# Kernel tuning notes

Hardware: AMD Instinct MI355X
Metric: run time of the kernel (lower is better)

The kernel has to match this reference:

```python
import jax, jax.numpy as jnp
import numpy as np

N = 4096     # batch of positions
E = 32       # descriptor buckets (experts)
NBLK = 12    # residual blocks per head


def _ln(x, g, b, eps=1e-5):
    m = x.mean(-1, keepdims=True)
    v = ((x - m) ** 2).mean(-1, keepdims=True)
    return (x - m) / jnp.sqrt(v + eps) * g + b


def _gelu(x):
    return jax.nn.gelu(x, approximate=False)  # torch nn.GELU default = exact erf


def setup_inputs() -> dict:
    key = jax.random.key(0)
    ks = iter(jax.random.split(key, 64))

    def nrm(shape, scale=0.05):
        return jax.random.normal(next(ks), shape, jnp.float32) * scale

    return {
        "piece_idx": jax.random.randint(next(ks), (N, 64), 0, 12),
        "side_flag": jax.random.randint(next(ks), (N,), 0, 2),
        "ep_file": jax.random.randint(next(ks), (N,), 0, 8),
        "castle_ms": jax.random.uniform(next(ks), (N, 4), jnp.float32),
        "fifty_a": jax.random.uniform(next(ks), (N,), jnp.float32),
        "descriptor_index": jax.random.randint(next(ks), (N,), 0, E),
        # per-bucket embedding tables, stacked on a leading expert axis
        "Wp_w": nrm((E, 64, 12, 32)), "Wp_b": nrm((E, 64, 12, 32)),
        "Wc_w": nrm((E, 4, 32)), "Wc_b": nrm((E, 4, 32)),
        "Wep_w": nrm((E, 8, 32)), "Wep_b": nrm((E, 8, 32)),
        "Wf_w": nrm((E, 2, 32)), "Wf_b": nrm((E, 2, 32)),
        # per-bucket MLP head params (weights stored as [in,out])
        "fc1_w": nrm((E, 2240, 256)), "fc1_b": nrm((E, 256)),
        "ln1_g": jnp.ones((E, 256)), "ln1_b": jnp.zeros((E, 256)),
        "fc2_w": nrm((E, 256, 32)), "fc2_b": nrm((E, 32)),
        "ln2_g": jnp.ones((E, 32)), "ln2_b": jnp.zeros((E, 32)),
        "blkA_w": nrm((NBLK, E, 32, 32)), "blkA_b": nrm((NBLK, E, 32)),
        "blkA_g": jnp.ones((NBLK, E, 32)), "blkA_be": jnp.zeros((NBLK, E, 32)),
        "blkB_w": nrm((NBLK, E, 32, 32)), "blkB_b": nrm((NBLK, E, 32)),
        "blkB_g": jnp.ones((NBLK, E, 32)), "blkB_be": jnp.zeros((NBLK, E, 32)),
        "out_w": nrm((E, 32, 51)), "out_b": nrm((E, 51)),
        "bins": jnp.linspace(0.0, 1.0, 51),
    }


def reference(piece_idx, side_flag, ep_file, castle_ms, fifty_a, descriptor_index,
              Wp_w, Wp_b, Wc_w, Wc_b, Wep_w, Wep_b, Wf_w, Wf_b,
              fc1_w, fc1_b, ln1_g, ln1_b, fc2_w, fc2_b, ln2_g, ln2_b,
              blkA_w, blkA_b, blkA_g, blkA_be, blkB_w, blkB_b, blkB_g, blkB_be,
              out_w, out_b, bins):
    desc = descriptor_index
    side = side_flag.astype(bool)
    n = piece_idx.shape[0]

    # ---- per-bucket, side-selected embedding gathers -> x_emb [N,2240] ----
    sq = jnp.arange(64)
    pc = jnp.maximum(piece_idx, 0)                                 # clamp -1 -> 0
    w_emb = Wp_w[desc[:, None], sq[None, :], pc]                    # [N,64,32]
    b_emb = Wp_b[desc[:, None], sq[None, :], pc]
    piece_emb = jnp.where(side[:, None, None], b_emb, w_emb)
    piece_emb = piece_emb * (piece_idx >= 0)[..., None].astype(piece_emb.dtype)
    pieces_vec = piece_emb.reshape(n, 2048)

    Wc = jnp.where(side[:, None, None], Wc_b[desc], Wc_w[desc])     # [N,4,32]
    castle_vec = (castle_ms[..., None] * Wc).reshape(n, 128)

    Wep = jnp.where(side[:, None, None], Wep_b[desc], Wep_w[desc])  # [N,8,32]
    epc = jnp.maximum(ep_file, 0)
    ep_vec = jnp.take_along_axis(Wep, epc[:, None, None], axis=1)[:, 0]
    ep_vec = ep_vec * (ep_file >= 0)[:, None].astype(ep_vec.dtype)

    Wf = jnp.where(side[:, None, None], Wf_b[desc], Wf_w[desc])     # [N,2,32]
    fifty_vec = (1.0 - fifty_a)[:, None] * Wf[:, 0] + fifty_a[:, None] * Wf[:, 1]

    x = jnp.concatenate([pieces_vec, castle_vec, ep_vec, fifty_vec], axis=1)  # [N,2240]

    # ---- expert-routed dense layer: all-expert GEMM + per-token select ----
    def dense_moe(h, W, b):
        ha = jnp.einsum('nd,edh->neh', h, W)                        # [N,E,out]
        hsel = jnp.take_along_axis(ha, desc[:, None, None], axis=1)[:, 0]
        return hsel + b[desc]

    h = _ln(_gelu(dense_moe(x, fc1_w, fc1_b)), ln1_g[desc], ln1_b[desc])   # [N,256]
    h = _ln(_gelu(dense_moe(h, fc2_w, fc2_b)), ln2_g[desc], ln2_b[desc])   # [N,32]

    def blk(carry, p):
        wA, bA, gA, beA, wB, bB, gB, beB = p
        y = _ln(_gelu(dense_moe(carry, wA, bA)), gA[desc], beA[desc])
        y = _ln(_gelu(dense_moe(y, wB, bB)), gB[desc], beB[desc])
        return carry + y, None

    h, _ = jax.lax.scan(blk, h, (blkA_w, blkA_b, blkA_g, blkA_be,
                                 blkB_w, blkB_b, blkB_g, blkB_be))

    logits = dense_moe(_gelu(h), out_w, out_b)                      # [N,51]
    p_win = jnp.sum(jax.nn.softmax(logits, axis=-1) * bins, axis=-1, keepdims=True)
    return logits, p_win
```

## Files before the change

### kernel.cpp

```cpp
#include <hip/hip_runtime.h>
#include <math.h>

#define N 4096
#define E 32
#define NBLK 12
#define D_IN 2240
#define H1 256
#define H2 32
#define NOUT 51
#define MT 16
#define NPAD (N + E*(MT-1))
#define NTILE (NPAD/MT)
#define KSPLIT 4
#define NROWS 4608
#define GMAX 96
#define NCONVBLK (35*4*E)

typedef short s8v __attribute__((ext_vector_type(8)));
typedef float f4v __attribute__((ext_vector_type(4)));

__device__ __forceinline__ float gelu(float x){
    return 0.5f * x * (1.0f + erff(x * 0.70710678118654752f));
}
__device__ __forceinline__ unsigned short f2bf(float f){
    unsigned int u = __float_as_uint(f);
    unsigned int r = (u + 0x7fffu + ((u >> 16) & 1u)) >> 16;
    return (unsigned short)r;
}
__device__ __forceinline__ float bflo(unsigned int u){ return __uint_as_float(u << 16); }
__device__ __forceinline__ float bfhi(unsigned int u){ return __uint_as_float(u & 0xffff0000u); }

template<int CTRL>
__device__ __forceinline__ float dppadd(float x){
    int y = __builtin_amdgcn_update_dpp(0, __float_as_int(x), CTRL, 0xF, 0xF, true);
    return x + __int_as_float(y);
}
__device__ __forceinline__ float red32(float x){
    x = dppadd<0x121>(x);
    x = dppadd<0x122>(x);
    x = dppadd<0x124>(x);
    x = dppadd<0x128>(x);
    int y = __builtin_amdgcn_ds_swizzle(__float_as_int(x), 0x401F);
    return x + __int_as_float(y);
}

__global__ void k_sort(const int* __restrict__ desc,
                       int* __restrict__ perm, int* __restrict__ tile_e,
                       int4* __restrict__ garr, int* __restrict__ ngroups){
    __shared__ int scnt[E];
    __shared__ int spoff[E+1];
    __shared__ int scur[E];
    int tid = threadIdx.x;
    if (tid < E) scnt[tid] = 0;
    __syncthreads();
    for (int n = tid; n < N; n += blockDim.x) atomicAdd(&scnt[desc[n]], 1);
    __syncthreads();
    if (tid == 0){
        int run = 0;
        for (int e = 0; e < E; e++){ spoff[e] = run; run += ((scnt[e] + MT - 1)/MT)*MT; }
        spoff[E] = run;
        int ng = 0;
        for (int e = 0; e < E; e++){
            int t0 = spoff[e]/MT, t1 = spoff[e+1]/MT;
            for (int t = t0; t < t1; t += 8){
                int nv = t1 - t; if (nv > 8) nv = 8;
                if (ng < GMAX) garr[ng] = make_int4(t, e, nv, 0);
                ng++;
            }
        }
        *ngroups = (ng > GMAX) ? GMAX : ng;
    }
    __syncthreads();
    if (tid < E) scur[tid] = spoff[tid];
    for (int p = tid; p < NPAD; p += blockDim.x) perm[p] = -1;
    __syncthreads();
    for (int n = tid; n < N; n += blockDim.x){
        int p = atomicAdd(&scur[desc[n]], 1);
        perm[p] = n;
    }
    for (int t = tid; t < NTILE; t += blockDim.x){
        int p0 = t*MT;
        int e = -1;
        if (p0 < spoff[E]){
            for (int q = 0; q < E; q++){
                if (p0 >= spoff[q] && p0 < spoff[q+1]){ e = q; break; }
            }
        }
        tile_e[t] = e;
    }
}

__global__ void k_prep(const int* __restrict__ perm,
                       const int* __restrict__ piece_idx,
                       const int* __restrict__ side_flag,
                       const int* __restrict__ ep_file,
                       const float* __restrict__ castle_ms,
                       const float* __restrict__ fifty_a,
                       const int* __restrict__ desc_idx,
                       const float* __restrict__ Wp_w, const float* __restrict__ Wp_b,
                       const float* __restrict__ Wc_w, const float* __restrict__ Wc_b,
                       const float* __restrict__ Wep_w, const float* __restrict__ Wep_b,
                       const float* __restrict__ Wf_w, const float* __restrict__ Wf_b,
                       unsigned short* __restrict__ xs,
                       const float* __restrict__ W1, unsigned short* __restrict__ Wt){
    __shared__ float lds[64][65];
    int tid = threadIdx.x;
    if (blockIdx.x >= NPAD){
        int b = blockIdx.x - NPAD;
        int kt = b % 35;
        int nt = (b / 35) & 3;
        int e  = b / 140;
        int k0 = kt*64, n0 = nt*64;
        int kk = tid >> 4, nn = (tid & 15) * 4;
        const float* src = W1 + ((size_t)e*D_IN + k0)*H1 + n0;
        #pragma unroll
        for (int r = 0; r < 4; r++){
            float4 v = *(const float4*)(src + (size_t)(kk + r*16)*H1 + nn);
            lds[kk + r*16][nn]   = v.x;
            lds[kk + r*16][nn+1] = v.y;
            lds[kk + r*16][nn+2] = v.z;
            lds[kk + r*16][nn+3] = v.w;
        }
        __syncthreads();
        int n = tid >> 2, kq = tid & 3;
        s8v p0, p1;
        #pragma unroll
        for (int j = 0; j < 8; j++) p0[j] = (short)f2bf(lds[kq*16 + j][n]);
        #pragma unroll
        for (int j = 0; j < 8; j++) p1[j] = (short)f2bf(lds[kq*16 + 8 + j][n]);
        unsigned short* dst = Wt + ((size_t)(e*H1 + n0 + n))*D_IN + k0 + kq*16;
        *(s8v*)dst       = p0;
        *(s8v*)(dst + 8) = p1;
        return;
    }
    int pos = blockIdx.x;
    int row = perm[pos];
    unsigned short* xr = xs + (size_t)pos * D_IN;
    if (row < 0){
        s8v z = {0,0,0,0,0,0,0,0};
        for (int t = tid; t < D_IN/8; t += blockDim.x) *(s8v*)(xr + t*8) = z;
        return;
    }
    int d = desc_idx[row];
    int s = side_flag[row];
    __shared__ int pidx[64];
    if (tid < 64) pidx[tid] = piece_idx[row*64 + tid];
    __syncthreads();
    const float* Wp  = s ? Wp_b  : Wp_w;
    const float* Wc  = s ? Wc_b  : Wc_w;
    const float* Wep = s ? Wep_b : Wep_w;
    const float* Wf  = s ? Wf_b  : Wf_w;
    int ep  = ep_file[row];
    int epc = ep > 0 ? ep : 0;
    float a = fifty_a[row];
    for (int t = tid; t < D_IN/8; t += blockDim.x){
        int i0 = t*8;
        float v[8];
        if (i0 < 2048){
            int sq = i0 >> 5, c0 = i0 & 31;
            int pc = pidx[sq];
            float msk = pc >= 0 ? 1.0f : 0.0f;
            int pcc = pc > 0 ? pc : 0;
            const float* base = Wp + (((size_t)d*64 + sq)*12 + pcc)*32 + c0;
            float4 a0 = *(const float4*)base;
            float4 a1 = *(const float4*)(base + 4);
            v[0]=a0.x*msk; v[1]=a0.y*msk; v[2]=a0.z*msk; v[3]=a0.w*msk;
            v[4]=a1.x*msk; v[5]=a1.y*msk; v[6]=a1.z*msk; v[7]=a1.w*msk;
        } else if (i0 < 2176){
            int j = i0 - 2048; int ci = j >> 5, c0 = j & 31;
            float cv = castle_ms[row*4 + ci];
            const float* base = Wc + ((size_t)d*4 + ci)*32 + c0;
            float4 a0 = *(const float4*)base;
            float4 a1 = *(const float4*)(base + 4);
            v[0]=a0.x*cv; v[1]=a0.y*cv; v[2]=a0.z*cv; v[3]=a0.w*cv;
            v[4]=a1.x*cv; v[5]=a1.y*cv; v[6]=a1.z*cv; v[7]=a1.w*cv;
        } else if (i0 < 2208){
            int c0 = i0 - 2176;
            float msk = ep >= 0 ? 1.0f : 0.0f;
            const float* base = Wep + ((size_t)d*8 + epc)*32 + c0;
            float4 a0 = *(const float4*)base;
            float4 a1 = *(const float4*)(base + 4);
            v[0]=a0.x*msk; v[1]=a0.y*msk; v[2]=a0.z*msk; v[3]=a0.w*msk;
            v[4]=a1.x*msk; v[5]=a1.y*msk; v[6]=a1.z*msk; v[7]=a1.w*msk;
        } else {
            int c0 = i0 - 2208;
            #pragma unroll
            for (int j = 0; j < 8; j++)
                v[j] = (1.0f - a) * Wf[(size_t)d*64 + c0 + j] + a * Wf[(size_t)d*64 + 32 + c0 + j];
        }
        s8v p;
        #pragma unroll
        for (int j = 0; j < 8; j++) p[j] = (short)f2bf(v[j]);
        *(s8v*)(xr + i0) = p;
    }
}

__launch_bounds__(256)
__global__ void k_fc1(const int4* __restrict__ garr, const int* __restrict__ ngroups,
                      const unsigned short* __restrict__ xs,
                      const unsigned short* __restrict__ Wt,
                      float* __restrict__ h1p){
    int g = blockIdx.x;
    if (g >= *ngroups) return;
    int4 gi = garr[g];
    int tile0 = gi.x, e = gi.y, nv = gi.z;
    int kc = blockIdx.y, nh = blockIdx.z;
    int kstart = (kc <= 2) ? kc*18 : 53;
    int nsteps = (kc < 2) ? 18 : 17;
    int lane = threadIdx.x & 63, wave = threadIdx.x >> 6;
    int quad = lane >> 4, l16 = lane & 15;
    int col0 = nh*128 + wave*32 + l16;
    const unsigned short* Ab = xs + (size_t)(tile0*MT + l16)*D_IN + quad*8;
    const unsigned short* B0 = Wt + ((size_t)e*H1 + col0)*D_IN + quad*8;
    const unsigned short* B1 = B0 + (size_t)16*D_IN;
    f4v acc[8][2];
    #pragma unroll
    for (int mt = 0; mt < 8; mt++){ acc[mt][0] = (f4v){0.f,0.f,0.f,0.f}; acc[mt][1] = (f4v){0.f,0.f,0.f,0.f}; }
    int kend = kstart + nsteps;
    #pragma unroll 2
    for (int s = kstart; s < kend; s++){
        int ko = s*32;
        s8v b0 = *(const s8v*)(B0 + ko);
        s8v b1 = *(const s8v*)(B1 + ko);
        #pragma unroll
        for (int mt = 0; mt < 8; mt++){
            s8v av = *(const s8v*)(Ab + (size_t)mt*MT*D_IN + ko);
            acc[mt][0] = __builtin_amdgcn_mfma_f32_16x16x32_bf16(av, b0, acc[mt][0], 0, 0, 0);
            acc[mt][1] = __builtin_amdgcn_mfma_f32_16x16x32_bf16(av, b1, acc[mt][1], 0, 0, 0);
        }
    }
    float* out = h1p + (size_t)kc*NROWS*H1;
    #pragma unroll
    for (int mt = 0; mt < 8; mt++){
        if (mt >= nv) break;
        int posb = (tile0 + mt)*MT + quad*4;
        #pragma unroll
        for (int r = 0; r < 4; r++){
            out[(size_t)(posb + r)*H1 + col0]      = acc[mt][0][r];
            out[(size_t)(posb + r)*H1 + col0 + 16] = acc[mt][1][r];
        }
    }
}

__launch_bounds__(256)
__global__ void k_tail(const int* __restrict__ tile_e, const int* __restrict__ perm,
                       const float* __restrict__ h1p, const float* __restrict__ b1,
                       const float* __restrict__ g1, const float* __restrict__ be1,
                       const float* __restrict__ W2, const float* __restrict__ b2,
                       const float* __restrict__ g2, const float* __restrict__ be2,
                       const float* __restrict__ Aw, const float* __restrict__ Abv,
                       const float* __restrict__ Ag, const float* __restrict__ Abe,
                       const float* __restrict__ Bw, const float* __restrict__ Bb,
                       const float* __restrict__ Bg, const float* __restrict__ Bbe,
                       const float* __restrict__ Ow, const float* __restrict__ Ob,
                       const float* __restrict__ bins,
                       float* __restrict__ out){
    int th = blockIdx.x;
    int t  = th >> 1;
    int r0 = (th & 1) * 8;
    int e = tile_e[t];
    if (e < 0) return;
    int tid = threadIdx.x;

    __shared__ __align__(16) float        shf[8*260];
    __shared__ __align__(16) unsigned int W2pk[4096];
    __shared__ __align__(16) float        vecs[NBLK*6*32];
    __shared__ __align__(16) unsigned int wbuf[2][1024];
    __shared__ __align__(16) float        sh2[8][36];
    __shared__ __align__(16) float        sh3[8][36];

    {
        const float* W2e = W2 + (size_t)e*H1*H2;
        for (int j = tid; j < 4096; j += 256){
            int h = j & 1, q = j >> 1, cc = q & 31, p2 = q >> 5;
            int k0 = 4*p2 + 2*h;
            unsigned int lo = f2bf(W2e[k0*32 + cc]);
            unsigned int hi = f2bf(W2e[(k0+1)*32 + cc]);
            W2pk[(p2*32 + cc)*2 + h] = lo | (hi << 16);
        }
    }
    for (int j = tid; j < NBLK*6*32; j += 256){
        int cc = j & 31, vi = (j >> 5) % 6, tb = j / 192;
        size_t wb = (size_t)tb*E + e;
        const float* src;
        switch(vi){ case 0: src=Abv; break; case 1: src=Ag; break; case 2: src=Abe; break;
                    case 3: src=Bb;  break; case 4: src=Bg; break; default: src=Bbe; }
        vecs[j] = src[wb*32 + cc];
    }
    {
        size_t base = (size_t)e*1024;
        #pragma unroll
        for (int k = 0; k < 4; k++){
            int s_all = k*256 + tid;
            int s = s_all & 511;
            int h = s & 1, q = s >> 1, cc = q & 31, p2 = q >> 5;
            int k0 = 4*p2 + 2*h;
            const float* src = (s_all >> 9) ? Bw : Aw;
            unsigned int lo = f2bf(src[base + k0*32 + cc]);
            unsigned int hi = f2bf(src[base + (k0+1)*32 + cc]);
            wbuf[0][s_all] = lo | (hi << 16);
        }
    }
    #pragma unroll
    for (int it = 0; it < 2; it++){
        int slot = it*256 + tid;
        int r = slot >> 6, c4 = (slot & 63) << 2;
        int row = t*MT + r0 + r;
        float4 v = {0.f,0.f,0.f,0.f};
        #pragma unroll
        for (int kc = 0; kc < KSPLIT; kc++){
            float4 p = *(const float4*)(h1p + ((size_t)kc*NROWS + row)*H1 + c4);
            v.x += p.x; v.y += p.y; v.z += p.z; v.w += p.w;
        }
        float4 bb = *(const float4*)(b1 + e*H1 + c4);
        shf[r*260 + c4]   = gelu(v.x + bb.x);
        shf[r*260 + c4+1] = gelu(v.y + bb.y);
        shf[r*260 + c4+2] = gelu(v.z + bb.z);
        shf[r*260 + c4+3] = gelu(v.w + bb.w);
    }
    __syncthreads();

    int m = tid >> 5, c = tid & 31;
    {
        float s = 0.f, s2 = 0.f;
        #pragma unroll
        for (int j = 0; j < 8; j++){
            float x = shf[m*260 + c + 32*j];
            s += x; s2 += x*x;
        }
        s  = red32(s);
        s2 = red32(s2);
        float mean = s * (1.0f/H1);
        float var  = s2 * (1.0f/H1) - mean*mean;
        float rs = rsqrtf(var + 1e-5f);
        #pragma unroll
        for (int j = 0; j < 8; j++){
            int k = c + 32*j;
            shf[m*260 + k] = (shf[m*260 + k] - mean) * rs * g1[e*H1 + k] + be1[e*H1 + k];
        }
    }
    float hv;
    {
        const uint2* W2p = (const uint2*)W2pk;
        float q0=0.f,q1=0.f,q2=0.f,q3=0.f;
        #pragma unroll 8
        for (int p2 = 0; p2 < 64; p2++){
            uint2 w = W2p[p2*32 + c];
            float4 h4 = *(const float4*)(shf + m*260 + p2*4);
            q0 = fmaf(h4.x, bflo(w.x), q0);
            q1 = fmaf(h4.y, bfhi(w.x), q1);
            q2 = fmaf(h4.z, bflo(w.y), q2);
            q3 = fmaf(h4.w, bfhi(w.y), q3);
        }
        float acc = (q0+q1) + (q2+q3) + b2[e*H2 + c];
        float y = gelu(acc);
        float s  = red32(y);
        float s2 = red32(y*y);
        float mean2 = s * (1.0f/H2);
        float var2  = s2 * (1.0f/H2) - mean2*mean2;
        hv = (y - mean2) * rsqrtf(var2 + 1e-5f) * g2[e*H2+c] + be2[e*H2+c];
    }

    int cur = 0;
    for (int tb = 0; tb < NBLK; tb++){
        float wfa[4], wfb[4];
        int tbn = tb + 1;
        if (tbn < NBLK){
            size_t base = ((size_t)tbn*E + e)*1024;
            #pragma unroll
            for (int k = 0; k < 4; k++){
                int s_all = k*256 + tid;
                int s = s_all & 511;
                int h = s & 1, q = s >> 1, cc = q & 31, p2 = q >> 5;
                int k0 = 4*p2 + 2*h;
                const float* src = (s_all >> 9) ? Bw : Aw;
                wfa[k] = src[base + k0*32 + cc];
                wfb[k] = src[base + (k0+1)*32 + cc];
            }
        }
        const float* vA = &vecs[tb*192];
        const uint2* WA = (const uint2*)&wbuf[cur][0];
        const uint2* WB = (const uint2*)&wbuf[cur][512];
        sh2[m][c] = hv;
        float q0=0.f,q1=0.f,q2=0.f,q3=0.f;
        #pragma unroll
        for (int p2 = 0; p2 < 8; p2++){
            uint2 w = WA[p2*32 + c];
            float4 h4 = *(const float4*)(&sh2[m][p2*4]);
            q0 = fmaf(h4.x, bflo(w.x), q0);
            q1 = fmaf(h4.y, bfhi(w.x), q1);
            q2 = fmaf(h4.z, bflo(w.y), q2);
            q3 = fmaf(h4.w, bfhi(w.y), q3);
        }
        float ya = (q0+q1) + (q2+q3) + vA[c];
        ya = gelu(ya);
        float sa  = red32(ya);
        float sa2 = red32(ya*ya);
        float ma = sa * (1.0f/H2);
        float va = sa2 * (1.0f/H2) - ma*ma;
        float yA = (ya - ma) * rsqrtf(va + 1e-5f) * vA[32+c] + vA[64+c];
        sh3[m][c] = yA;
        q0=0.f; q1=0.f; q2=0.f; q3=0.f;
        #pragma unroll
        for (int p2 = 0; p2 < 8; p2++){
            uint2 w = WB[p2*32 + c];
            float4 h4 = *(const float4*)(&sh3[m][p2*4]);
            q0 = fmaf(h4.x, bflo(w.x), q0);
            q1 = fmaf(h4.y, bfhi(w.x), q1);
            q2 = fmaf(h4.z, bflo(w.y), q2);
            q3 = fmaf(h4.w, bfhi(w.y), q3);
        }
        float yb = (q0+q1) + (q2+q3) + vA[96+c];
        yb = gelu(yb);
        float sb  = red32(yb);
        float sb2 = red32(yb*yb);
        float mb = sb * (1.0f/H2);
        float vb = sb2 * (1.0f/H2) - mb*mb;
        hv += (yb - mb) * rsqrtf(vb + 1e-5f) * vA[128+c] + vA[160+c];
        if (tbn < NBLK){
            #pragma unroll
            for (int k = 0; k < 4; k++){
                int s_all = k*256 + tid;
                unsigned int lo = f2bf(wfa[k]);
                unsigned int hi = f2bf(wfb[k]);
                wbuf[cur^1][s_all] = lo | (hi << 16);
            }
        }
        cur ^= 1;
        __syncthreads();
    }

    sh2[m][c] = gelu(hv);
    __syncthreads();
    int wave = tid >> 6, lane = tid & 63;
    const float* W = Ow + (size_t)e*32*NOUT;
    for (int rr = wave; rr < 8; rr += 4){
        int orow = perm[t*MT + r0 + rr];
        if (orow < 0) continue;
        float acc = (lane < NOUT) ? Ob[e*NOUT + lane] : -INFINITY;
        #pragma unroll
        for (int k = 0; k < 32; k++){
            float gk = sh2[rr][k];
            if (lane < NOUT) acc = fmaf(gk, W[k*NOUT + lane], acc);
        }
        if (lane < NOUT) out[(size_t)orow*NOUT + lane] = acc;
        float mx = acc;
        #pragma unroll
        for (int o = 32; o > 0; o >>= 1) mx = fmaxf(mx, __shfl_xor(mx, o));
        float pp = (lane < NOUT) ? expf(acc - mx) : 0.0f;
        float sum = pp;
        float pb = (lane < NOUT) ? pp * bins[lane] : 0.0f;
        float sb = pb;
        #pragma unroll
        for (int o = 32; o > 0; o >>= 1){ sum += __shfl_xor(sum, o); sb += __shfl_xor(sb, o); }
        if (lane == 0) out[(size_t)N*NOUT + orow] = sb / sum;
    }
}

extern "C" void kernel_launch(void* const* d_in, const int* in_sizes, int n_in,
                              void* d_out, int out_size, void* d_ws, size_t ws_size,
                              hipStream_t stream){
    const int*   piece_idx = (const int*)d_in[0];
    const int*   side_flag = (const int*)d_in[1];
    const int*   ep_file   = (const int*)d_in[2];
    const float* castle_ms = (const float*)d_in[3];
    const float* fifty_a   = (const float*)d_in[4];
    const int*   desc      = (const int*)d_in[5];
    const float* Wp_w  = (const float*)d_in[6];
    const float* Wp_b  = (const float*)d_in[7];
    const float* Wc_w  = (const float*)d_in[8];
    const float* Wc_b  = (const float*)d_in[9];
    const float* Wep_w = (const float*)d_in[10];
    const float* Wep_b = (const float*)d_in[11];
    const float* Wf_w  = (const float*)d_in[12];
    const float* Wf_b  = (const float*)d_in[13];
    const float* fc1_w = (const float*)d_in[14];
    const float* fc1_b = (const float*)d_in[15];
    const float* ln1_g = (const float*)d_in[16];
    const float* ln1_b = (const float*)d_in[17];
    const float* fc2_w = (const float*)d_in[18];
    const float* fc2_b = (const float*)d_in[19];
    const float* ln2_g = (const float*)d_in[20];
    const float* ln2_b = (const float*)d_in[21];
    const float* blkA_w  = (const float*)d_in[22];
    const float* blkA_b  = (const float*)d_in[23];
    const float* blkA_g  = (const float*)d_in[24];
    const float* blkA_be = (const float*)d_in[25];
    const float* blkB_w  = (const float*)d_in[26];
    const float* blkB_b  = (const float*)d_in[27];
    const float* blkB_g  = (const float*)d_in[28];
    const float* blkB_be = (const float*)d_in[29];
    const float* out_w = (const float*)d_in[30];
    const float* out_b = (const float*)d_in[31];
    const float* bins  = (const float*)d_in[32];

    char* wsp = (char*)d_ws;
    auto alloc = [&](size_t bytes){ void* p = (void*)wsp; wsp += (bytes + 255) & ~(size_t)255; return p; };
    int*            perm    = (int*)            alloc((size_t)NPAD*4);
    int*            tile_e  = (int*)            alloc((size_t)NTILE*4);
    int4*           garr    = (int4*)           alloc((size_t)GMAX*16);
    int*            ngroups = (int*)            alloc(256);
    unsigned short* Wt      = (unsigned short*) alloc((size_t)E*H1*D_IN*2);
    unsigned short* xs      = (unsigned short*) alloc((size_t)(NPAD+128)*D_IN*2);
    float*          h1p     = (float*)          alloc((size_t)KSPLIT*NROWS*H1*4);

    k_sort<<<1, 256, 0, stream>>>(desc, perm, tile_e, garr, ngroups);
    k_prep<<<NPAD + NCONVBLK, 256, 0, stream>>>(perm, piece_idx, side_flag, ep_file,
                                                castle_ms, fifty_a, desc,
                                                Wp_w, Wp_b, Wc_w, Wc_b,
                                                Wep_w, Wep_b, Wf_w, Wf_b,
                                                xs, fc1_w, Wt);
    k_fc1<<<dim3(GMAX, KSPLIT, 2), 256, 0, stream>>>(garr, ngroups, xs, Wt, h1p);
    k_tail<<<NTILE*2, 256, 0, stream>>>(tile_e, perm, h1p, fc1_b, ln1_g, ln1_b,
                                        fc2_w, fc2_b, ln2_g, ln2_b,
                                        blkA_w, blkA_b, blkA_g, blkA_be,
                                        blkB_w, blkB_b, blkB_g, blkB_be,
                                        out_w, out_b, bins, (float*)d_out);
}
```

Baseline: 300.6 us.

## Fuse sort into prep, gather rows via perm, convert fc1 weights in-GEMM

Merges the single-block sort kernel into the prep kernel's block 0 and builds embedding rows in original order, so fc1 gathers A rows through perm, with padded slots pointing at a zeroed sentinel row. The separate fp32-to-bf16 transpose pass over the fc1 weights and its workspace are removed. The fc1 GEMM now loads fp32 weight tiles into LDS each k-step and converts them to bf16 there, which adds two barriers per step and repeated conversion work. This only saves launches and weight-conversion traffic if the extra per-step synchronisation stays cheap. There is also a risk, since k_fc1 reads perm, tile_e and garr written by block 0 of the same kernel launch before it. Stream ordering between launches makes that safe.

Measured after the change: 282.6 us. 1.06x faster.

```diff
diff --git a/kernel.cpp b/kernel.cpp
--- a/kernel.cpp
+++ b/kernel.cpp
@@ -14,7 +14,6 @@
 #define KSPLIT 4
 #define NROWS 4608
 #define GMAX 96
-#define NCONVBLK (35*4*E)
 
 typedef short s8v __attribute__((ext_vector_type(8)));
 typedef float f4v __attribute__((ext_vector_type(4)));
@@ -44,54 +43,7 @@
     return x + __int_as_float(y);
 }
 
-__global__ void k_sort(const int* __restrict__ desc,
-                       int* __restrict__ perm, int* __restrict__ tile_e,
-                       int4* __restrict__ garr, int* __restrict__ ngroups){
-    __shared__ int scnt[E];
-    __shared__ int spoff[E+1];
-    __shared__ int scur[E];
-    int tid = threadIdx.x;
-    if (tid < E) scnt[tid] = 0;
-    __syncthreads();
-    for (int n = tid; n < N; n += blockDim.x) atomicAdd(&scnt[desc[n]], 1);
-    __syncthreads();
-    if (tid == 0){
-        int run = 0;
-        for (int e = 0; e < E; e++){ spoff[e] = run; run += ((scnt[e] + MT - 1)/MT)*MT; }
-        spoff[E] = run;
-        int ng = 0;
-        for (int e = 0; e < E; e++){
-            int t0 = spoff[e]/MT, t1 = spoff[e+1]/MT;
-            for (int t = t0; t < t1; t += 8){
-                int nv = t1 - t; if (nv > 8) nv = 8;
-                if (ng < GMAX) garr[ng] = make_int4(t, e, nv, 0);
-                ng++;
-            }
-        }
-        *ngroups = (ng > GMAX) ? GMAX : ng;
-    }
-    __syncthreads();
-    if (tid < E) scur[tid] = spoff[tid];
-    for (int p = tid; p < NPAD; p += blockDim.x) perm[p] = -1;
-    __syncthreads();
-    for (int n = tid; n < N; n += blockDim.x){
-        int p = atomicAdd(&scur[desc[n]], 1);
-        perm[p] = n;
-    }
-    for (int t = tid; t < NTILE; t += blockDim.x){
-        int p0 = t*MT;
-        int e = -1;
-        if (p0 < spoff[E]){
-            for (int q = 0; q < E; q++){
-                if (p0 >= spoff[q] && p0 < spoff[q+1]){ e = q; break; }
-            }
-        }
-        tile_e[t] = e;
-    }
-}
-
-__global__ void k_prep(const int* __restrict__ perm,
-                       const int* __restrict__ piece_idx,
+__global__ void k_prep(const int* __restrict__ piece_idx,
                        const int* __restrict__ side_flag,
                        const int* __restrict__ ep_file,
                        const float* __restrict__ castle_ms,
@@ -102,45 +54,57 @@
                        const float* __restrict__ Wep_w, const float* __restrict__ Wep_b,
                        const float* __restrict__ Wf_w, const float* __restrict__ Wf_b,
                        unsigned short* __restrict__ xs,
-                       const float* __restrict__ W1, unsigned short* __restrict__ Wt){
-    __shared__ float lds[64][65];
+                       int* __restrict__ perm, int* __restrict__ tile_e,
+                       int4* __restrict__ garr, int* __restrict__ ngroups){
     int tid = threadIdx.x;
-    if (blockIdx.x >= NPAD){
-        int b = blockIdx.x - NPAD;
-        int kt = b % 35;
-        int nt = (b / 35) & 3;
-        int e  = b / 140;
-        int k0 = kt*64, n0 = nt*64;
-        int kk = tid >> 4, nn = (tid & 15) * 4;
-        const float* src = W1 + ((size_t)e*D_IN + k0)*H1 + n0;
-        #pragma unroll
-        for (int r = 0; r < 4; r++){
-            float4 v = *(const float4*)(src + (size_t)(kk + r*16)*H1 + nn);
-            lds[kk + r*16][nn]   = v.x;
-            lds[kk + r*16][nn+1] = v.y;
-            lds[kk + r*16][nn+2] = v.z;
-            lds[kk + r*16][nn+3] = v.w;
-        }
-        __syncthreads();
-        int n = tid >> 2, kq = tid & 3;
-        s8v p0, p1;
-        #pragma unroll
-        for (int j = 0; j < 8; j++) p0[j] = (short)f2bf(lds[kq*16 + j][n]);
-        #pragma unroll
-        for (int j = 0; j < 8; j++) p1[j] = (short)f2bf(lds[kq*16 + 8 + j][n]);
-        unsigned short* dst = Wt + ((size_t)(e*H1 + n0 + n))*D_IN + k0 + kq*16;
-        *(s8v*)dst       = p0;
-        *(s8v*)(dst + 8) = p1;
+    if (blockIdx.x == 0){
+        __shared__ int scnt[E];
+        __shared__ int spoff[E+1];
+        __shared__ int scur[E];
+        if (tid < E) scnt[tid] = 0;
+        __syncthreads();
+        for (int n = tid; n < N; n += blockDim.x) atomicAdd(&scnt[desc_idx[n]], 1);
+        __syncthreads();
+        if (tid == 0){
+            int run = 0;
+            for (int e = 0; e < E; e++){ spoff[e] = run; run += ((scnt[e] + MT - 1)/MT)*MT; }
+            spoff[E] = run;
+            int ng = 0;
+            for (int e = 0; e < E; e++){
+                int t0 = spoff[e]/MT, t1 = spoff[e+1]/MT;
+                for (int t = t0; t < t1; t += 8){
+                    int nv = t1 - t; if (nv > 8) nv = 8;
+                    if (ng < GMAX) garr[ng] = make_int4(t, e, nv, 0);
+                    ng++;
+                }
+            }
+            *ngroups = (ng > GMAX) ? GMAX : ng;
+        }
+        __syncthreads();
+        if (tid < E) scur[tid] = spoff[tid];
+        for (int p = tid; p < NPAD + 64; p += blockDim.x) perm[p] = -1;
+        __syncthreads();
+        for (int n = tid; n < N; n += blockDim.x){
+            int p = atomicAdd(&scur[desc_idx[n]], 1);
+            perm[p] = n;
+        }
+        for (int t = tid; t < NTILE; t += blockDim.x){
+            int p0 = t*MT;
+            int e = -1;
+            if (p0 < spoff[E]){
+                for (int q = 0; q < E; q++){
+                    if (p0 >= spoff[q] && p0 < spoff[q+1]){ e = q; break; }
+                }
+            }
+            tile_e[t] = e;
+        }
+        s8v z = {0,0,0,0,0,0,0,0};
+        for (int i = tid; i < D_IN/8; i += blockDim.x)
+            *(s8v*)(xs + (size_t)N*D_IN + i*8) = z;
         return;
     }
-    int pos = blockIdx.x;
-    int row = perm[pos];
-    unsigned short* xr = xs + (size_t)pos * D_IN;
-    if (row < 0){
-        s8v z = {0,0,0,0,0,0,0,0};
-        for (int t = tid; t < D_IN/8; t += blockDim.x) *(s8v*)(xr + t*8) = z;
-        return;
-    }
+    int row = blockIdx.x - 1;
+    unsigned short* xr = xs + (size_t)row * D_IN;
     int d = desc_idx[row];
     int s = side_flag[row];
     __shared__ int pidx[64];
@@ -198,7 +162,8 @@
 __launch_bounds__(256)
 __global__ void k_fc1(const int4* __restrict__ garr, const int* __restrict__ ngroups,
                       const unsigned short* __restrict__ xs,
-                      const unsigned short* __restrict__ Wt,
+                      const int* __restrict__ perm,
+                      const float* __restrict__ W1,
                       float* __restrict__ h1p){
     int g = blockIdx.x;
     if (g >= *ngroups) return;
@@ -207,28 +172,58 @@
     int kc = blockIdx.y, nh = blockIdx.z;
     int kstart = (kc <= 2) ? kc*18 : 53;
     int nsteps = (kc < 2) ? 18 : 17;
-    int lane = threadIdx.x & 63, wave = threadIdx.x >> 6;
+    int tid = threadIdx.x;
+    int lane = tid & 63, wave = tid >> 6;
     int quad = lane >> 4, l16 = lane & 15;
-    int col0 = nh*128 + wave*32 + l16;
-    const unsigned short* Ab = xs + (size_t)(tile0*MT + l16)*D_IN + quad*8;
-    const unsigned short* B0 = Wt + ((size_t)e*H1 + col0)*D_IN + quad*8;
-    const unsigned short* B1 = B0 + (size_t)16*D_IN;
+
+    __shared__ float bst[32][133];
+
+    const unsigned short* Arow[8];
+    #pragma unroll
+    for (int mt = 0; mt < 8; mt++){
+        int p = perm[(tile0 + mt)*MT + l16];
+        if (p < 0) p = N;
+        Arow[mt] = xs + (size_t)p*D_IN + quad*8;
+    }
+
+    const float* Wb = W1 + (size_t)e*D_IN*H1 + nh*128;
+    int kk0 = tid >> 5;
+    int nq4 = (tid & 31) << 2;
+    int cl0 = wave*32 + l16;
+    int cl1 = cl0 + 16;
+
     f4v acc[8][2];
     #pragma unroll
     for (int mt = 0; mt < 8; mt++){ acc[mt][0] = (f4v){0.f,0.f,0.f,0.f}; acc[mt][1] = (f4v){0.f,0.f,0.f,0.f}; }
+
     int kend = kstart + nsteps;
-    #pragma unroll 2
     for (int s = kstart; s < kend; s++){
-        int ko = s*32;
-        s8v b0 = *(const s8v*)(B0 + ko);
-        s8v b1 = *(const s8v*)(B1 + ko);
+        int kb = s*32;
+        #pragma unroll
+        for (int p = 0; p < 4; p++){
+            int kk = p*8 + kk0;
+            float4 v = *(const float4*)(Wb + (size_t)(kb + kk)*H1 + nq4);
+            bst[kk][nq4]   = v.x;
+            bst[kk][nq4+1] = v.y;
+            bst[kk][nq4+2] = v.z;
+            bst[kk][nq4+3] = v.w;
+        }
+        __syncthreads();
+        s8v b0, b1;
+        #pragma unroll
+        for (int j = 0; j < 8; j++){
+            b0[j] = (short)f2bf(bst[quad*8 + j][cl0]);
+            b1[j] = (short)f2bf(bst[quad*8 + j][cl1]);
+        }
         #pragma unroll
         for (int mt = 0; mt < 8; mt++){
-            s8v av = *(const s8v*)(Ab + (size_t)mt*MT*D_IN + ko);
+            s8v av = *(const s8v*)(Arow[mt] + kb);
             acc[mt][0] = __builtin_amdgcn_mfma_f32_16x16x32_bf16(av, b0, acc[mt][0], 0, 0, 0);
             acc[mt][1] = __builtin_amdgcn_mfma_f32_16x16x32_bf16(av, b1, acc[mt][1], 0, 0, 0);
         }
-    }
+        __syncthreads();
+    }
+    int col0 = nh*128 + wave*32 + l16;
     float* out = h1p + (size_t)kc*NROWS*H1;
     #pragma unroll
     for (int mt = 0; mt < 8; mt++){
@@ -496,21 +491,19 @@
 
     char* wsp = (char*)d_ws;
     auto alloc = [&](size_t bytes){ void* p = (void*)wsp; wsp += (bytes + 255) & ~(size_t)255; return p; };
-    int*            perm    = (int*)            alloc((size_t)NPAD*4);
+    int*            perm    = (int*)            alloc((size_t)(NPAD+128)*4);
     int*            tile_e  = (int*)            alloc((size_t)NTILE*4);
     int4*           garr    = (int4*)           alloc((size_t)GMAX*16);
     int*            ngroups = (int*)            alloc(256);
-    unsigned short* Wt      = (unsigned short*) alloc((size_t)E*H1*D_IN*2);
-    unsigned short* xs      = (unsigned short*) alloc((size_t)(NPAD+128)*D_IN*2);
+    unsigned short* xs      = (unsigned short*) alloc((size_t)(N+128)*D_IN*2);
     float*          h1p     = (float*)          alloc((size_t)KSPLIT*NROWS*H1*4);
 
-    k_sort<<<1, 256, 0, stream>>>(desc, perm, tile_e, garr, ngroups);
-    k_prep<<<NPAD + NCONVBLK, 256, 0, stream>>>(perm, piece_idx, side_flag, ep_file,
-                                                castle_ms, fifty_a, desc,
-                                                Wp_w, Wp_b, Wc_w, Wc_b,
-                                                Wep_w, Wep_b, Wf_w, Wf_b,
-                                                xs, fc1_w, Wt);
-    k_fc1<<<dim3(GMAX, KSPLIT, 2), 256, 0, stream>>>(garr, ngroups, xs, Wt, h1p);
+    k_prep<<<1 + N, 256, 0, stream>>>(piece_idx, side_flag, ep_file,
+                                      castle_ms, fifty_a, desc,
+                                      Wp_w, Wp_b, Wc_w, Wc_b,
+                                      Wep_w, Wep_b, Wf_w, Wf_b,
+                                      xs, perm, tile_e, garr, ngroups);
+    k_fc1<<<dim3(GMAX, KSPLIT, 2), 256, 0, stream>>>(garr, ngroups, xs, perm, fc1_w, h1p);
     k_tail<<<NTILE*2, 256, 0, stream>>>(tile_e, perm, h1p, fc1_b, ln1_g, ln1_b,
                                         fc2_w, fc2_b, ln2_g, ln2_b,
                                         blkA_w, blkA_b, blkA_g, blkA_be,
```
